# Optimization experiments

Measured on AMD Instinct MI355X. Metric: run time of the kernel, lower is better.

The kernel has to match this reference:

```python
import jax, jax.numpy as jnp
import numpy as np

B, S, DIM, H = 2, 2048, 1536, 12
HD = DIM // H  # 128
EPS = 1e-6


def setup_inputs() -> dict:
    key = jax.random.key(0)
    ks = jax.random.split(key, 6)
    x = jax.random.normal(ks[0], (B, S, DIM), dtype=jnp.float32)
    # RoPE rotation as (cos, sin) pairs: shape [S, 1, HD//2, 2]
    inv = 1.0 / (10000.0 ** (np.arange(0, HD, 2, dtype=np.float32) / HD))
    ang = np.arange(S, dtype=np.float32)[:, None] * inv[None, :]  # [S, HD//2]
    freqs = jnp.asarray(np.stack([np.cos(ang), np.sin(ang)], axis=-1))[:, None, :, :]
    def lin(k):
        return jax.random.normal(k, (DIM, DIM), dtype=jnp.float32) * 0.02
    wq, wk, wv, wo = lin(ks[1]), lin(ks[2]), lin(ks[3]), lin(ks[4])
    zb = jnp.zeros((DIM,), dtype=jnp.float32)
    ones = jnp.ones((DIM,), dtype=jnp.float32)
    return dict(x=x, freqs=freqs,
                wq=wq, bq=zb, wk=wk, bk=zb, wv=wv, bv=zb, wo=wo, bo=zb,
                gq=ones, gk=ones, timestep=500)


def reference(x, freqs, wq, bq, wk, bk, wv, bv, wo, bo, gq, gk, timestep):
    b, s, dim = x.shape

    def rms(z, g):
        zf = z.astype(jnp.float32)
        n = zf * jax.lax.rsqrt(jnp.mean(zf * zf, axis=-1, keepdims=True) + EPS)
        return n.astype(z.dtype) * g

    def rope(t):
        # [b,s,dim] -> [b,s,H,HD//2,2] pairs; complex multiply by freqs
        tp = t.reshape(b, s, H, HD // 2, 2)
        tr, ti = tp[..., 0], tp[..., 1]
        fr = freqs[None, ..., 0]  # [1,s,1,HD//2] broadcasts over batch & heads
        fi = freqs[None, ..., 1]
        out = jnp.stack([tr * fr - ti * fi, tr * fi + ti * fr], axis=-1)
        return out.reshape(b, s, dim)

    q = rope(rms(x @ wq.T + bq, gq))
    k = rope(rms(x @ wk.T + bk, gk))
    v = x @ wv.T + bv

    qh = q.reshape(b, s, H, HD).transpose(0, 2, 1, 3)
    kh = k.reshape(b, s, H, HD).transpose(0, 2, 1, 3)
    vh = v.reshape(b, s, H, HD).transpose(0, 2, 1, 3)
    scores = jnp.einsum('bhqd,bhkd->bhqk', qh, kh) / np.float32(np.sqrt(HD))
    attn = jax.nn.softmax(scores, axis=-1)
    out = jnp.einsum('bhqk,bhkd->bhqd', attn, vh)
    out = out.transpose(0, 2, 1, 3).reshape(b, s, dim)
    return out @ wo.T + bo
```

## Files before the change

### kernel.cpp

```cpp
#include <hip/hip_runtime.h>
#include <hip/hip_bf16.h>


#define BQ  2
#define SQ  2048
#define DIMQ 1536
#define HQ  12
#define HDQ 128
#define MTOK 4096
#define KDIM 1536

typedef __attribute__((ext_vector_type(8))) short short8;
typedef __attribute__((ext_vector_type(4))) float f32x4;
typedef __attribute__((ext_vector_type(16))) float f32x16;
typedef __attribute__((ext_vector_type(8))) unsigned short u16x8;

typedef __attribute__((address_space(1))) const void global_cvoid;
typedef __attribute__((address_space(3))) void lds_void;

__device__ __forceinline__ float bf2f(unsigned int u) {
    return __uint_as_float(u << 16);
}
__device__ __forceinline__ unsigned short f2bf(float f) {
    unsigned int u = __float_as_uint(f);
    u += 0x7fffu + ((u >> 16) & 1u);
    return (unsigned short)(u >> 16);
}
__device__ __forceinline__ void gload_lds16(const void* g, void* l) {
    __builtin_amdgcn_global_load_lds((global_cvoid*)g, (lds_void*)l, 16, 0, 0);
}
__device__ __forceinline__ unsigned int cvtpk_bf16(float lo, float hi) {
    unsigned int r;
    asm("v_cvt_pk_bf16_f32 %0, %1, %2" : "=v"(r) : "v"(lo), "v"(hi));
    return r;
}

#define VMCNT(n) asm volatile("s_waitcnt vmcnt(" #n ")" ::: "memory")
#define MEMFENCE() asm volatile("" ::: "memory")

__global__ __launch_bounds__(256)
void cast_all(const float* __restrict__ x,
              const float* __restrict__ wq, const float* __restrict__ wk,
              const float* __restrict__ wv, const float* __restrict__ wo,
              unsigned short* __restrict__ Xb,
              unsigned short* __restrict__ Wqkv,
              unsigned short* __restrict__ Wob)
{
    const int NX = 1572864, NW = 589824;
    int i = blockIdx.x * blockDim.x + threadIdx.x;
    int stride = gridDim.x * blockDim.x;
    for (; i < NX + 4 * NW; i += stride) {
        const float* s; unsigned short* d; int off;
        if (i < NX) { s = x; d = Xb; off = i; }
        else {
            int j = i - NX;
            int seg = j / NW;
            off = j - seg * NW;
            s = (seg == 0) ? wq : (seg == 1) ? wk : (seg == 2) ? wv : wo;
            d = (seg < 3) ? (Wqkv + seg * 2359296) : Wob;
        }
        float4 v = ((const float4*)s)[off];
        unsigned short a = f2bf(v.x), b = f2bf(v.y), c = f2bf(v.z), e = f2bf(v.w);
        unsigned int lo = (unsigned int)a | ((unsigned int)b << 16);
        unsigned int hi = (unsigned int)c | ((unsigned int)e << 16);
        ((uint2*)d)[off] = make_uint2(lo, hi);
    }
}

template<int MODE>
__global__ __launch_bounds__(256)
void gemm_bt(const unsigned short* __restrict__ A,
             const unsigned short* __restrict__ Bm,
             unsigned short* __restrict__ oQ,
             unsigned short* __restrict__ oK,
             unsigned short* __restrict__ oV,
             const float* __restrict__ biasq,
             const float* __restrict__ biask,
             const float* __restrict__ biasv,
             float* __restrict__ oF,
             const float* __restrict__ biaso)
{
    __shared__ unsigned short ldsA[128 * 64];
    __shared__ unsigned short ldsB[128 * 64];
    const int m0 = blockIdx.x * 128;
    const int n0 = blockIdx.y * 128;
    const int t = threadIdx.x;
    const int lane = t & 63;
    const int wid = t >> 6;
    const int wr = (wid >> 1) * 64;
    const int wc = (wid & 1) * 64;
    const int lr = lane & 15;
    const int lk = lane >> 4;

    f32x4 acc[4][4] = {};

    #pragma unroll 1
    for (int kt = 0; kt < KDIM; kt += 64) {
        #pragma unroll
        for (int i = 0; i < 4; ++i) {
            const int off = i * 4096 + wid * 1024 + lane * 16;
            const int r = off >> 7;
            const int c = (off >> 4) & 7;
            const int csw = (c ^ (r & 7)) << 3;
            gload_lds16(A + (size_t)(m0 + r) * KDIM + kt + csw,
                        (char*)ldsA + i * 4096 + wid * 1024);
            gload_lds16(Bm + (size_t)(n0 + r) * KDIM + kt + csw,
                        (char*)ldsB + i * 4096 + wid * 1024);
        }
        __syncthreads();

        #pragma unroll
        for (int kk = 0; kk < 2; ++kk) {
            short8 af[4], bf[4];
            #pragma unroll
            for (int mi = 0; mi < 4; ++mi) {
                int row = wr + mi * 16 + lr;
                int ch = (kk * 4 + lk) ^ (row & 7);
                af[mi] = *(const short8*)((const char*)ldsA + row * 128 + ch * 16);
            }
            #pragma unroll
            for (int ni = 0; ni < 4; ++ni) {
                int row = wc + ni * 16 + lr;
                int ch = (kk * 4 + lk) ^ (row & 7);
                bf[ni] = *(const short8*)((const char*)ldsB + row * 128 + ch * 16);
            }
            #pragma unroll
            for (int mi = 0; mi < 4; ++mi)
                #pragma unroll
                for (int ni = 0; ni < 4; ++ni)
                    acc[mi][ni] = __builtin_amdgcn_mfma_f32_16x16x32_bf16(
                        af[mi], bf[ni], acc[mi][ni], 0, 0, 0);
        }
        __syncthreads();
    }

    if (MODE == 0) {
        const int seg = n0 / 1536;
        unsigned short* op = (seg == 0) ? oQ : (seg == 1 ? oK : oV);
        const float* bp = (seg == 0) ? biasq : (seg == 1 ? biask : biasv);
        const int nl0 = n0 - seg * 1536;
        #pragma unroll
        for (int mi = 0; mi < 4; ++mi)
            #pragma unroll
            for (int ni = 0; ni < 4; ++ni)
                #pragma unroll
                for (int j = 0; j < 4; ++j) {
                    int row = m0 + wr + mi * 16 + lk * 4 + j;
                    int col = nl0 + wc + ni * 16 + lr;
                    op[(size_t)row * 1536 + col] = f2bf(acc[mi][ni][j] + bp[col]);
                }
    } else {
        #pragma unroll
        for (int mi = 0; mi < 4; ++mi)
            #pragma unroll
            for (int ni = 0; ni < 4; ++ni)
                #pragma unroll
                for (int j = 0; j < 4; ++j) {
                    int row = m0 + wr + mi * 16 + lk * 4 + j;
                    int col = n0 + wc + ni * 16 + lr;
                    oF[(size_t)row * 1536 + col] = acc[mi][ni][j] + biaso[col];
                }
    }
}

__global__ __launch_bounds__(256)
void rmsnorm_rope(unsigned short* __restrict__ T,
                  const float* __restrict__ g,
                  const float* __restrict__ freqs)
{
    const int token = blockIdx.x;
    const int s = token & (SQ - 1);
    unsigned int* row = (unsigned int*)(T + (size_t)token * DIMQ);
    const int t = threadIdx.x;
    const int lane = t & 63, wid = t >> 6;

    float pr[3], pi[3];
    float ss = 0.f;
    #pragma unroll
    for (int q = 0; q < 3; ++q) {
        unsigned int v = row[t + q * 256];
        float a = bf2f(v & 0xffffu);
        float b = bf2f(v >> 16);
        pr[q] = a; pi[q] = b;
        ss += a * a + b * b;
    }
    ss += __shfl_xor(ss, 32); ss += __shfl_xor(ss, 16); ss += __shfl_xor(ss, 8);
    ss += __shfl_xor(ss, 4);  ss += __shfl_xor(ss, 2);  ss += __shfl_xor(ss, 1);
    __shared__ float red[4];
    if (lane == 0) red[wid] = ss;
    __syncthreads();
    float tot = red[0] + red[1] + red[2] + red[3];
    float sc = rsqrtf(tot * (1.0f / 1536.0f) + 1e-6f);

    #pragma unroll
    for (int q = 0; q < 3; ++q) {
        int p = t + q * 256;
        int ph = p & 63;
        float fr = freqs[s * 128 + ph * 2];
        float fi = freqs[s * 128 + ph * 2 + 1];
        float nr = pr[q] * sc * g[2 * p];
        float ni = pi[q] * sc * g[2 * p + 1];
        float outr = nr * fr - ni * fi;
        float outi = nr * fi + ni * fr;
        row[p] = (unsigned int)f2bf(outr) | ((unsigned int)f2bf(outi) << 16);
    }
}

__global__ __launch_bounds__(256)
void vtrans(const unsigned short* __restrict__ V, unsigned short* __restrict__ Vt)
{
    __shared__ unsigned short tile[64][72];
    const int s0 = blockIdx.x * 64;
    const int d0 = blockIdx.y * 64;
    const int bh = blockIdx.z;
    const int b = bh / HQ, h = bh % HQ;
    const int t = threadIdx.x;

    #pragma unroll
    for (int i = 0; i < 2; ++i) {
        int cid = i * 256 + t;
        int r = cid >> 3, c = cid & 7;
        u16x8 v = *(const u16x8*)(V + (size_t)(b * SQ + s0 + r) * DIMQ + h * HDQ + d0 + c * 8);
        #pragma unroll
        for (int e = 0; e < 8; ++e) tile[r][c * 8 + e] = v[e];
    }
    __syncthreads();
    #pragma unroll
    for (int i = 0; i < 2; ++i) {
        int cid = i * 256 + t;
        int rd = cid >> 3, c = cid & 7;
        u16x8 w;
        #pragma unroll
        for (int e = 0; e < 8; ++e) w[e] = tile[c * 8 + e][rd];
        *(u16x8*)(Vt + (size_t)(bh * HDQ + d0 + rd) * SQ + s0 + c * 8) = w;
    }
}

__global__ __launch_bounds__(64, 2)
void attn(const unsigned short* __restrict__ Q,
          const unsigned short* __restrict__ Kb,
          const unsigned short* __restrict__ Vt,
          unsigned short* __restrict__ Ao)
{
    __shared__ char smem[24576];
    char* Kl0 = smem;
    char* Kl1 = smem + 8192;
    char* Vl  = smem + 16384;

    const int fid = blockIdx.x;
    const int xcd = fid & 7;
    const int slot = fid >> 3;
    const int bh = xcd * 3 + (slot >> 6);
    const int sblk = slot & 63;
    const int b = bh / HQ, h = bh % HQ;
    const int s0 = sblk * 32;

    const int lane = threadIdx.x;
    const int l31 = lane & 31, hi = lane >> 5;
    const float CE = 0.12751879f;
    const float THR = 90.5f;

    const unsigned short* Kbase = Kb + (size_t)(b * SQ) * DIMQ + h * HDQ;
    const unsigned short* Vbase = Vt + (size_t)(bh * HDQ) * SQ;

    short8 qf[8];
    {
        const unsigned short* qp = Q + (size_t)(b * SQ + s0 + l31) * DIMQ + h * HDQ;
        #pragma unroll
        for (int kc = 0; kc < 8; ++kc)
            qf[kc] = *(const short8*)(qp + kc * 16 + hi * 8);
    }
    MEMFENCE();
    #pragma unroll
    for (int i = 0; i < 8; ++i) {
        const int off = i * 1024 + lane * 16;
        int r = off >> 8, c = (off >> 4) & 15;
        gload_lds16(Kbase + (size_t)r * DIMQ + ((c ^ (r & 7)) << 3), Kl0 + i * 1024);
    }
    VMCNT(8);

    char* kcur = Kl0;
    char* knxt = Kl1;
    float mrun = -1e30f, lsum = 0.f, nm = 1e30f;
    f32x16 oacc[4] = {};

    #pragma unroll 1
    for (int kv0 = 0; kv0 < SQ; kv0 += 32) {
        #pragma unroll
        for (int i = 0; i < 8; ++i) {
            const int off = i * 1024 + lane * 16;
            int r = off >> 6, c = (off >> 4) & 3;
            gload_lds16(Vbase + (size_t)r * SQ + kv0 + ((c ^ ((r >> 1) & 3)) << 3),
                        Vl + i * 1024);
        }
        MEMFENCE();
        const int kvn = (kv0 + 32 < SQ) ? kv0 + 32 : kv0;
        #pragma unroll
        for (int i = 0; i < 8; ++i) {
            const int off = i * 1024 + lane * 16;
            int r = off >> 8, c = (off >> 4) & 15;
            gload_lds16(Kbase + (size_t)(kvn + r) * DIMQ + ((c ^ (r & 7)) << 3),
                        knxt + i * 1024);
        }

        VMCNT(16);

        f32x16 sa = {}, sb = {};
        const int rb = l31 * 256;
        const int rx = l31 & 7;
        #pragma unroll
        for (int kc = 0; kc < 4; ++kc) {
            short8 kf = *(const short8*)(kcur + rb + (((kc * 2 + hi) ^ rx) << 4));
            sa = __builtin_amdgcn_mfma_f32_32x32x16_bf16(kf, qf[kc], sa, 0, 0, 0);
        }
        #pragma unroll
        for (int kc = 4; kc < 8; ++kc) {
            short8 kf = *(const short8*)(kcur + rb + (((kc * 2 + hi) ^ rx) << 4));
            sb = __builtin_amdgcn_mfma_f32_32x32x16_bf16(kf, qf[kc], sb, 0, 0, 0);
        }
        f32x16 s;
        #pragma unroll
        for (int r = 0; r < 16; ++r) s[r] = sa[r] + sb[r];

        float mt[8];
        #pragma unroll
        for (int r = 0; r < 8; ++r) mt[r] = fmaxf(s[r], s[r + 8]);
        #pragma unroll
        for (int st = 4; st > 0; st >>= 1)
            #pragma unroll
            for (int r = 0; r < 4; ++r)
                if (r < st) mt[r] = fmaxf(mt[r], mt[r + st]);
        float tm = fmaxf(mt[0], __shfl_xor(mt[0], 32));
        if (!__all(tm <= mrun + THR)) {
            float mnew = fmaxf(mrun, tm);
            float al = __builtin_amdgcn_exp2f((mrun - mnew) * CE);
            lsum *= al;
            #pragma unroll
            for (int dt = 0; dt < 4; ++dt)
                #pragma unroll
                for (int r = 0; r < 16; ++r) oacc[dt][r] *= al;
            mrun = mnew;
            nm = -mrun * CE;
        }
        float rs = 0.f;
        #pragma unroll
        for (int r = 0; r < 16; ++r) {
            float p = __builtin_amdgcn_exp2f(__builtin_fmaf(s[r], CE, nm));
            s[r] = p; rs += p;
        }
        rs += __shfl_xor(rs, 32);
        lsum += rs;

        unsigned int A0 = cvtpk_bf16(s[0], s[1]),  A1 = cvtpk_bf16(s[2], s[3]);
        unsigned int B0 = cvtpk_bf16(s[4], s[5]),  B1 = cvtpk_bf16(s[6], s[7]);
        unsigned int C0 = cvtpk_bf16(s[8], s[9]),  C1 = cvtpk_bf16(s[10], s[11]);
        unsigned int D0 = cvtpk_bf16(s[12], s[13]), D1 = cvtpk_bf16(s[14], s[15]);
        unsigned int xA0 = __shfl_xor(A0, 32), xA1 = __shfl_xor(A1, 32);
        unsigned int xB0 = __shfl_xor(B0, 32), xB1 = __shfl_xor(B1, 32);
        unsigned int xC0 = __shfl_xor(C0, 32), xC1 = __shfl_xor(C1, 32);
        unsigned int xD0 = __shfl_xor(D0, 32), xD1 = __shfl_xor(D1, 32);
        union { unsigned int w[4]; short8 v; } pf0, pf1;
        pf0.w[0] = hi ? xB0 : A0;  pf0.w[1] = hi ? xB1 : A1;
        pf0.w[2] = hi ? B0 : xA0;  pf0.w[3] = hi ? B1 : xA1;
        pf1.w[0] = hi ? xD0 : C0;  pf1.w[1] = hi ? xD1 : C1;
        pf1.w[2] = hi ? D0 : xC0;  pf1.w[3] = hi ? D1 : xC1;

        VMCNT(8);

        #pragma unroll
        for (int dt = 0; dt < 4; ++dt) {
            const int drow = dt * 32 + l31;
            const int sw = (drow >> 1) & 3;
            short8 v0 = *(const short8*)(Vl + drow * 64 + ((hi ^ sw) << 4));
            short8 v1 = *(const short8*)(Vl + drow * 64 + (((2 + hi) ^ sw) << 4));
            oacc[dt] = __builtin_amdgcn_mfma_f32_32x32x16_bf16(v0, pf0.v, oacc[dt], 0, 0, 0);
            oacc[dt] = __builtin_amdgcn_mfma_f32_32x32x16_bf16(v1, pf1.v, oacc[dt], 0, 0, 0);
        }

        char* tp = kcur; kcur = knxt; knxt = tp;
    }

    const float rls = 1.0f / lsum;
    char* Ot = Vl;
    #pragma unroll
    for (int dt = 0; dt < 4; ++dt)
        #pragma unroll
        for (int rp = 0; rp < 8; ++rp) {
            const int r = 2 * rp;
            float v0 = oacc[dt][r] * rls;
            float v1 = oacc[dt][r + 1] * rls;
            int d = dt * 32 + (r & 3) + 8 * (r >> 2) + 4 * hi;
            unsigned int w = (unsigned int)f2bf(v0) | ((unsigned int)f2bf(v1) << 16);
            int addr = l31 * 256 + (((d >> 3) ^ (l31 & 7)) << 4) + (d & 7) * 2;
            *(unsigned int*)(Ot + addr) = w;
        }
    #pragma unroll
    for (int ii = 0; ii < 8; ++ii) {
        int task = ii * 64 + lane;
        int q = task >> 4, c = task & 15;
        u16x8 vv = *(const u16x8*)(Ot + q * 256 + ((c ^ (q & 7)) << 4));
        int tok = b * SQ + s0 + q;
        *(u16x8*)(Ao + (size_t)tok * DIMQ + h * HDQ + c * 8) = vv;
    }
}

extern "C" void kernel_launch(void* const* d_in, const int* in_sizes, int n_in,
                              void* d_out, int out_size, void* d_ws, size_t ws_size,
                              hipStream_t stream) {
    (void)in_sizes; (void)n_in; (void)out_size; (void)ws_size;
    const float* x     = (const float*)d_in[0];
    const float* freqs = (const float*)d_in[1];
    const float* wq = (const float*)d_in[2];
    const float* bq = (const float*)d_in[3];
    const float* wk = (const float*)d_in[4];
    const float* bk = (const float*)d_in[5];
    const float* wv = (const float*)d_in[6];
    const float* bv = (const float*)d_in[7];
    const float* wo = (const float*)d_in[8];
    const float* bo = (const float*)d_in[9];
    const float* gq = (const float*)d_in[10];
    const float* gk = (const float*)d_in[11];
    float* out = (float*)d_out;

    char* w = (char*)d_ws;
    unsigned short* Xb   = (unsigned short*)(w);
    unsigned short* Wqkv = (unsigned short*)(w + 12582912);
    unsigned short* Wob  = (unsigned short*)(w + 26738688);
    unsigned short* Qb   = (unsigned short*)(w + 31457280);
    unsigned short* Kbuf = (unsigned short*)(w + 44040192);
    unsigned short* Vb   = (unsigned short*)(w + 56623104);
    unsigned short* Vt   = (unsigned short*)(w + 69206016);
    unsigned short* Ao   = Xb;

    cast_all<<<2048, 256, 0, stream>>>(x, wq, wk, wv, wo, Xb, Wqkv, Wob);

    gemm_bt<0><<<dim3(32, 36), 256, 0, stream>>>(
        Xb, Wqkv, Qb, Kbuf, Vb, bq, bk, bv, nullptr, nullptr);

    rmsnorm_rope<<<4096, 256, 0, stream>>>(Qb,   gq, freqs);
    rmsnorm_rope<<<4096, 256, 0, stream>>>(Kbuf, gk, freqs);
    vtrans<<<dim3(32, 2, 24), 256, 0, stream>>>(Vb, Vt);

    attn<<<1536, 64, 0, stream>>>(Qb, Kbuf, Vt, Ao);

    gemm_bt<1><<<dim3(32, 12), 256, 0, stream>>>(
        Ao, Wob, nullptr, nullptr, nullptr, nullptr, nullptr, nullptr, out, bo);
}
```

Before: 255.4 us.

## Split attention KV range in two and share K/V tiles across two waves

The attention kernel now uses 128-thread blocks. Two waves handle 64 query rows and share the cooperatively loaded K/V LDS tiles, with barriers between stages. Each block covers half of the KV sequence, and a new combine kernel merges the two partial outputs using the stored max and sum statistics. This is meant to halve the global-to-LDS traffic per query row and raise parallelism, at the cost of an extra kernel launch, a bf16 round-trip for the partial outputs, and block-wide barriers; setprio hints are added around the MFMA sections.

```diff
diff --git a/kernel.cpp b/kernel.cpp
--- a/kernel.cpp
+++ b/kernel.cpp
@@ -18,6 +18,8 @@
 typedef __attribute__((address_space(1))) const void global_cvoid;
 typedef __attribute__((address_space(3))) void lds_void;
 
+__device__ const float CEc = 0.12751879f;
+
 __device__ __forceinline__ float bf2f(unsigned int u) {
     return __uint_as_float(u << 16);
 }
@@ -37,6 +39,9 @@
 
 #define VMCNT(n) asm volatile("s_waitcnt vmcnt(" #n ")" ::: "memory")
 #define MEMFENCE() asm volatile("" ::: "memory")
+#define BARRIER() do { asm volatile("" ::: "memory"); \
+                       __builtin_amdgcn_s_barrier();  \
+                       asm volatile("" ::: "memory"); } while (0)
 
 __global__ __launch_bounds__(256)
 void cast_all(const float* __restrict__ x,
@@ -236,11 +241,13 @@
     }
 }
 
-__global__ __launch_bounds__(64, 2)
+__global__ __launch_bounds__(128)
 void attn(const unsigned short* __restrict__ Q,
           const unsigned short* __restrict__ Kb,
           const unsigned short* __restrict__ Vt,
-          unsigned short* __restrict__ Ao)
+          unsigned short* __restrict__ Op0,
+          unsigned short* __restrict__ Op1,
+          float* __restrict__ ml)
 {
     __shared__ char smem[24576];
     char* Kl0 = smem;
@@ -251,13 +258,17 @@
     const int xcd = fid & 7;
     const int slot = fid >> 3;
     const int bh = xcd * 3 + (slot >> 6);
-    const int sblk = slot & 63;
+    const int r64 = slot & 63;
+    const int qt = r64 >> 1;
+    const int sp = r64 & 1;
     const int b = bh / HQ, h = bh % HQ;
-    const int s0 = sblk * 32;
-
-    const int lane = threadIdx.x;
+
+    const int t = threadIdx.x;
+    const int lane = t & 63, wid = t >> 6;
     const int l31 = lane & 31, hi = lane >> 5;
-    const float CE = 0.12751879f;
+    const int s0q = qt * 64 + wid * 32;
+    const int f = (bh * 32 + qt) * 2 + wid;
+    const int kvbeg = sp * 1024, kvend = kvbeg + 1024;
     const float THR = 90.5f;
 
     const unsigned short* Kbase = Kb + (size_t)(b * SQ) * DIMQ + h * HDQ;
@@ -265,19 +276,21 @@
 
     short8 qf[8];
     {
-        const unsigned short* qp = Q + (size_t)(b * SQ + s0 + l31) * DIMQ + h * HDQ;
+        const unsigned short* qp = Q + (size_t)(b * SQ + s0q + l31) * DIMQ + h * HDQ;
         #pragma unroll
         for (int kc = 0; kc < 8; ++kc)
             qf[kc] = *(const short8*)(qp + kc * 16 + hi * 8);
     }
     MEMFENCE();
     #pragma unroll
-    for (int i = 0; i < 8; ++i) {
-        const int off = i * 1024 + lane * 16;
+    for (int i = 0; i < 4; ++i) {
+        const int j = wid * 4 + i;
+        const int off = j * 1024 + lane * 16;
         int r = off >> 8, c = (off >> 4) & 15;
-        gload_lds16(Kbase + (size_t)r * DIMQ + ((c ^ (r & 7)) << 3), Kl0 + i * 1024);
-    }
-    VMCNT(8);
+        gload_lds16(Kbase + (size_t)(kvbeg + r) * DIMQ + ((c ^ (r & 7)) << 3),
+                    Kl0 + j * 1024);
+    }
+    VMCNT(4);
 
     char* kcur = Kl0;
     char* knxt = Kl1;
@@ -285,29 +298,33 @@
     f32x16 oacc[4] = {};
 
     #pragma unroll 1
-    for (int kv0 = 0; kv0 < SQ; kv0 += 32) {
-        #pragma unroll
-        for (int i = 0; i < 8; ++i) {
-            const int off = i * 1024 + lane * 16;
+    for (int kv0 = kvbeg; kv0 < kvend; kv0 += 32) {
+        #pragma unroll
+        for (int i = 0; i < 4; ++i) {
+            const int j = wid * 4 + i;
+            const int off = j * 1024 + lane * 16;
             int r = off >> 6, c = (off >> 4) & 3;
             gload_lds16(Vbase + (size_t)r * SQ + kv0 + ((c ^ ((r >> 1) & 3)) << 3),
-                        Vl + i * 1024);
+                        Vl + j * 1024);
         }
         MEMFENCE();
         const int kvn = (kv0 + 32 < SQ) ? kv0 + 32 : kv0;
         #pragma unroll
-        for (int i = 0; i < 8; ++i) {
-            const int off = i * 1024 + lane * 16;
+        for (int i = 0; i < 4; ++i) {
+            const int j = wid * 4 + i;
+            const int off = j * 1024 + lane * 16;
             int r = off >> 8, c = (off >> 4) & 15;
             gload_lds16(Kbase + (size_t)(kvn + r) * DIMQ + ((c ^ (r & 7)) << 3),
-                        knxt + i * 1024);
-        }
-
-        VMCNT(16);
+                        knxt + j * 1024);
+        }
+
+        VMCNT(8);
+        BARRIER();
 
         f32x16 sa = {}, sb = {};
         const int rb = l31 * 256;
         const int rx = l31 & 7;
+        __builtin_amdgcn_s_setprio(1);
         #pragma unroll
         for (int kc = 0; kc < 4; ++kc) {
             short8 kf = *(const short8*)(kcur + rb + (((kc * 2 + hi) ^ rx) << 4));
@@ -318,6 +335,7 @@
             short8 kf = *(const short8*)(kcur + rb + (((kc * 2 + hi) ^ rx) << 4));
             sb = __builtin_amdgcn_mfma_f32_32x32x16_bf16(kf, qf[kc], sb, 0, 0, 0);
         }
+        __builtin_amdgcn_s_setprio(0);
         f32x16 s;
         #pragma unroll
         for (int r = 0; r < 16; ++r) s[r] = sa[r] + sb[r];
@@ -333,22 +351,21 @@
         float tm = fmaxf(mt[0], __shfl_xor(mt[0], 32));
         if (!__all(tm <= mrun + THR)) {
             float mnew = fmaxf(mrun, tm);
-            float al = __builtin_amdgcn_exp2f((mrun - mnew) * CE);
+            float al = __builtin_amdgcn_exp2f((mrun - mnew) * CEc);
             lsum *= al;
             #pragma unroll
             for (int dt = 0; dt < 4; ++dt)
                 #pragma unroll
                 for (int r = 0; r < 16; ++r) oacc[dt][r] *= al;
             mrun = mnew;
-            nm = -mrun * CE;
+            nm = -mrun * CEc;
         }
         float rs = 0.f;
         #pragma unroll
         for (int r = 0; r < 16; ++r) {
-            float p = __builtin_amdgcn_exp2f(__builtin_fmaf(s[r], CE, nm));
+            float p = __builtin_amdgcn_exp2f(__builtin_fmaf(s[r], CEc, nm));
             s[r] = p; rs += p;
         }
-        rs += __shfl_xor(rs, 32);
         lsum += rs;
 
         unsigned int A0 = cvtpk_bf16(s[0], s[1]),  A1 = cvtpk_bf16(s[2], s[3]);
@@ -365,8 +382,10 @@
         pf1.w[0] = hi ? xD0 : C0;  pf1.w[1] = hi ? xD1 : C1;
         pf1.w[2] = hi ? D0 : xC0;  pf1.w[3] = hi ? D1 : xC1;
 
-        VMCNT(8);
-
+        VMCNT(4);
+        BARRIER();
+
+        __builtin_amdgcn_s_setprio(1);
         #pragma unroll
         for (int dt = 0; dt < 4; ++dt) {
             const int drow = dt * 32 + l31;
@@ -376,30 +395,79 @@
             oacc[dt] = __builtin_amdgcn_mfma_f32_32x32x16_bf16(v0, pf0.v, oacc[dt], 0, 0, 0);
             oacc[dt] = __builtin_amdgcn_mfma_f32_32x32x16_bf16(v1, pf1.v, oacc[dt], 0, 0, 0);
         }
+        __builtin_amdgcn_s_setprio(0);
+
+        BARRIER();
 
         char* tp = kcur; kcur = knxt; knxt = tp;
     }
 
-    const float rls = 1.0f / lsum;
-    char* Ot = Vl;
+    float ltot = lsum + __shfl_xor(lsum, 32);
+    float rnl = 1.0f / ltot;
+    unsigned short* Op = sp ? Op1 : Op0;
+    #pragma unroll
+    for (int dt = 0; dt < 4; ++dt) {
+        unsigned int w[8];
+        #pragma unroll
+        for (int j = 0; j < 8; ++j)
+            w[j] = (unsigned int)f2bf(oacc[dt][2 * j] * rnl)
+                 | ((unsigned int)f2bf(oacc[dt][2 * j + 1] * rnl) << 16);
+        *(uint4*)(Op + (size_t)f * 4096 + (dt * 2 + 0) * 512 + lane * 8) =
+            make_uint4(w[0], w[1], w[2], w[3]);
+        *(uint4*)(Op + (size_t)f * 4096 + (dt * 2 + 1) * 512 + lane * 8) =
+            make_uint4(w[4], w[5], w[6], w[7]);
+    }
+    ml[(size_t)(sp * 1536 + f) * 128 + lane] = mrun;
+    ml[(size_t)(sp * 1536 + f) * 128 + 64 + lane] = ltot;
+}
+
+__global__ __launch_bounds__(256)
+void attn_combine(const unsigned short* __restrict__ Op0,
+                  const unsigned short* __restrict__ Op1,
+                  const float* __restrict__ ml,
+                  unsigned short* __restrict__ Ao)
+{
+    __shared__ char smem[32768];
+    const int f = blockIdx.x * 4 + (threadIdx.x >> 6);
+    const int lane = threadIdx.x & 63;
+    const int l31 = lane & 31, hi = lane >> 5;
+    const int bh = f >> 6, qt = (f >> 1) & 31, wid = f & 1;
+    const int b = bh / HQ, h = bh % HQ;
+    const int s0q = qt * 64 + wid * 32;
+
+    float m0 = ml[(size_t)f * 128 + lane];
+    float l0 = ml[(size_t)f * 128 + 64 + lane];
+    float m1 = ml[(size_t)(1536 + f) * 128 + lane];
+    float l1 = ml[(size_t)(1536 + f) * 128 + 64 + lane];
+    float ms = fmaxf(m0, m1);
+    float w0 = __builtin_amdgcn_exp2f((m0 - ms) * CEc) * l0;
+    float w1 = __builtin_amdgcn_exp2f((m1 - ms) * CEc) * l1;
+    float rL = 1.0f / (w0 + w1);
+    float a0 = w0 * rL, a1 = w1 * rL;
+
+    char* Ot = smem + (threadIdx.x >> 6) * 8192;
     #pragma unroll
     for (int dt = 0; dt < 4; ++dt)
         #pragma unroll
-        for (int rp = 0; rp < 8; ++rp) {
-            const int r = 2 * rp;
-            float v0 = oacc[dt][r] * rls;
-            float v1 = oacc[dt][r + 1] * rls;
-            int d = dt * 32 + (r & 3) + 8 * (r >> 2) + 4 * hi;
-            unsigned int w = (unsigned int)f2bf(v0) | ((unsigned int)f2bf(v1) << 16);
-            int addr = l31 * 256 + (((d >> 3) ^ (l31 & 7)) << 4) + (d & 7) * 2;
-            *(unsigned int*)(Ot + addr) = w;
+        for (int hf = 0; hf < 2; ++hf) {
+            u16x8 o0 = *(const u16x8*)(Op0 + (size_t)f * 4096 + (dt * 2 + hf) * 512 + lane * 8);
+            u16x8 o1 = *(const u16x8*)(Op1 + (size_t)f * 4096 + (dt * 2 + hf) * 512 + lane * 8);
+            #pragma unroll
+            for (int j = 0; j < 4; ++j) {
+                int r = hf * 8 + 2 * j;
+                float v0 = a0 * bf2f((unsigned short)o0[2 * j])     + a1 * bf2f((unsigned short)o1[2 * j]);
+                float v1 = a0 * bf2f((unsigned short)o0[2 * j + 1]) + a1 * bf2f((unsigned short)o1[2 * j + 1]);
+                int d = dt * 32 + (r & 3) + 8 * (r >> 2) + 4 * hi;
+                unsigned int w = (unsigned int)f2bf(v0) | ((unsigned int)f2bf(v1) << 16);
+                *(unsigned int*)(Ot + l31 * 256 + (((d >> 3) ^ (l31 & 7)) << 4) + (d & 7) * 2) = w;
+            }
         }
     #pragma unroll
     for (int ii = 0; ii < 8; ++ii) {
         int task = ii * 64 + lane;
         int q = task >> 4, c = task & 15;
         u16x8 vv = *(const u16x8*)(Ot + q * 256 + ((c ^ (q & 7)) << 4));
-        int tok = b * SQ + s0 + q;
+        int tok = b * SQ + s0q + q;
         *(u16x8*)(Ao + (size_t)tok * DIMQ + h * HDQ + c * 8) = vv;
     }
 }
@@ -431,6 +499,9 @@
     unsigned short* Vb   = (unsigned short*)(w + 56623104);
     unsigned short* Vt   = (unsigned short*)(w + 69206016);
     unsigned short* Ao   = Xb;
+    unsigned short* Op0  = Wqkv;
+    float*          mlbf = (float*)(w + 25165824);
+    unsigned short* Op1  = Vb;
 
     cast_all<<<2048, 256, 0, stream>>>(x, wq, wk, wv, wo, Xb, Wqkv, Wob);
 
@@ -441,7 +512,8 @@
     rmsnorm_rope<<<4096, 256, 0, stream>>>(Kbuf, gk, freqs);
     vtrans<<<dim3(32, 2, 24), 256, 0, stream>>>(Vb, Vt);
 
-    attn<<<1536, 64, 0, stream>>>(Qb, Kbuf, Vt, Ao);
+    attn<<<1536, 128, 0, stream>>>(Qb, Kbuf, Vt, Op0, Op1, mlbf);
+    attn_combine<<<384, 256, 0, stream>>>(Op0, Op1, mlbf, Ao);
 
     gemm_bt<1><<<dim3(32, 12), 256, 0, stream>>>(
         Ao, Wob, nullptr, nullptr, nullptr, nullptr, nullptr, nullptr, out, bo);
```

After: 259.2 us. Within noise of the previous version (+1.5%).
